# Optimization experiments

Measured on AMD Instinct MI355X. Metric: run time of the kernel, lower is better.

## Reference

```python
import jax, jax.numpy as jnp
import numpy as np

VOCAB = 32000
EMB = 128
HID = 256
NCLS = 8
B, S = 256, 512


def setup_inputs() -> dict:
    key = jax.random.key(0)
    ks = jax.random.split(key, 10)
    tokens = jax.random.randint(ks[0], (B, S), 0, VOCAB)
    emb = jax.random.normal(ks[1], (VOCAB, EMB), jnp.float32) * 0.02
    # LSTM params per direction: Wi [EMB,4H] (no bias, like flax dense_i),
    # Wh [H,4H] + bh [4H] (flax dense_h carries the bias). Gate order: i,f,g,o.
    si = 1.0 / np.sqrt(EMB)
    sh = 1.0 / np.sqrt(HID)
    Wi_f = jax.random.normal(ks[2], (EMB, 4 * HID), jnp.float32) * si
    Wh_f = jax.random.normal(ks[3], (HID, 4 * HID), jnp.float32) * sh
    b_f = jnp.zeros((4 * HID,), jnp.float32)
    Wi_b = jax.random.normal(ks[4], (EMB, 4 * HID), jnp.float32) * si
    Wh_b = jax.random.normal(ks[5], (HID, 4 * HID), jnp.float32) * sh
    b_b = jnp.zeros((4 * HID,), jnp.float32)
    Wd = jax.random.normal(ks[6], (2 * HID, NCLS), jnp.float32) * (1.0 / np.sqrt(2 * HID))
    bd = jnp.zeros((NCLS,), jnp.float32)
    return {"tokens": tokens, "emb": emb, "Wi_f": Wi_f, "Wh_f": Wh_f, "b_f": b_f,
            "Wi_b": Wi_b, "Wh_b": Wh_b, "b_b": b_b, "Wd": Wd, "bd": bd, "train": 0}


def _lstm_final_c(xs, Wi, Wh, bh):
    # xs: [B, S, E]. Returns final cell state c_S: [B, H].
    bsz = xs.shape[0]
    # Precompute input projections for all steps: [S, B, 4H]
    x_proj = jnp.einsum('bse,eg->sbg', xs, Wi) + bh

    def step(carry, xp_t):
        c, h = carry
        z = xp_t + h @ Wh  # [B, 4H]
        i, f, g, o = jnp.split(z, 4, axis=-1)
        c = jax.nn.sigmoid(f) * c + jax.nn.sigmoid(i) * jnp.tanh(g)
        h = jax.nn.sigmoid(o) * jnp.tanh(c)
        return (c, h), None

    init = (jnp.zeros((bsz, HID), xs.dtype), jnp.zeros((bsz, HID), xs.dtype))
    (c, h), _ = jax.lax.scan(step, init, x_proj)
    return c


def reference(tokens, emb, Wi_f, Wh_f, b_f, Wi_b, Wh_b, b_b, Wd, bd, train):
    x = emb[tokens]                       # [B, S, E]
    c_fwd = _lstm_final_c(x, Wi_f, Wh_f, b_f)
    c_bwd = _lstm_final_c(jnp.flip(x, axis=1), Wi_b, Wh_b, b_b)
    feat = jnp.concatenate([c_fwd, c_bwd], axis=-1)  # [B, 2H]
    # Dropout is deterministic (train=False) -> identity.
    return feat @ Wd + bd                 # [B, NCLS]
```

## Files before the change

kernel.cpp:

```cpp
#include <hip/hip_runtime.h>
#include <hip/hip_bf16.h>


typedef __attribute__((ext_vector_type(8))) short bf16x8;
typedef __attribute__((ext_vector_type(4))) float f32x4;

#define S_LEN 512

#define XF_OFF   0ULL
#define XF_SZ    (512ULL*16*4*64*16)
#define WHF_OFF  (XF_OFF + XF_SZ)
#define WHF_SZ   (2ULL*8*8*8*64*16)
#define WIF_OFF  (WHF_OFF + WHF_SZ)
#define WIF_SZ   (2ULL*8*4*8*64*16)
#define FEAT_OFF (WIF_OFF + WIF_SZ)
#define FEAT_SZ  (256ULL*512*4)
#define FLAG_OFF (FEAT_OFF + FEAT_SZ)
#define WS_NEED  (FLAG_OFF + 16)

__device__ __forceinline__ short f2bf(float f){
  union { float f; unsigned u; } v; v.f = f;
  unsigned u = v.u;
  u += 0x7fffu + ((u >> 16) & 1u);
  return (short)(u >> 16);
}
__device__ __forceinline__ float fsig(float x){
  float t = __builtin_amdgcn_exp2f(-1.44269504f * x);
  return __builtin_amdgcn_rcpf(1.0f + t);
}
__device__ __forceinline__ float ftanh(float x){
  float t = __builtin_amdgcn_exp2f(2.88539008f * x);
  return 1.0f - 2.0f * __builtin_amdgcn_rcpf(1.0f + t);
}
__device__ __forceinline__ int pack2(float a, float b){
  return (int)(unsigned short)f2bf(a) | ((int)(unsigned short)f2bf(b) << 16);
}
__device__ __forceinline__ int koff(int flag, int h, int j){
  return flag ? (8*h + j) : (j < 4 ? 4*h + j : 16 + 4*h + (j-4));
}
__device__ __forceinline__ bf16x8 loadA(const short* p, int colbase, int h, int flag){
  if (flag){
    return *(const bf16x8*)(p + colbase + 8*h);
  } else {
    short4 lo = *(const short4*)(p + colbase + 4*h);
    short4 hi = *(const short4*)(p + colbase + 16 + 4*h);
    bf16x8 r;
    r[0]=lo.x; r[1]=lo.y; r[2]=lo.z; r[3]=lo.w;
    r[4]=hi.x; r[5]=hi.y; r[6]=hi.z; r[7]=hi.w;
    return r;
  }
}

__device__ __noinline__ void spin_units(int n){
  float x = 1.5f;
  for (int i=0; i<n*300; i++) x = __builtin_amdgcn_rcpf(x + 1.0f);
  asm volatile("" :: "v"(x));
}
__global__ __launch_bounds__(64) void probe_kernel(char* ws){
  int l = threadIdx.x;
  float dref[4]; int n = l & 15;
  #pragma unroll
  for (int r=0;r<4;r++){
    int m = 4*(l>>4) + r; float s = 0.f;
    for (int k=0;k<32;k++)
      s += (0.25f*(float)((m*7+k*3)%5-2)) * (0.125f*(float)((k*5+n*11)%7-3));
    dref[r] = s;
  }
  f32x4 zero = {0.f,0.f,0.f,0.f};
  int bad[2];
  #pragma unroll
  for (int cand=0; cand<2; cand++){
    bf16x8 a, b;
    #pragma unroll
    for (int j=0;j<8;j++){
      int k = koff(cand, l>>4, j);
      a[j] = f2bf(0.25f*(float)(((l&15)*7+k*3)%5-2));
      b[j] = f2bf(0.125f*(float)((k*5+(l&15)*11)%7-3));
    }
    f32x4 d = __builtin_amdgcn_mfma_f32_16x16x32_bf16(a,b,zero,0,0,0);
    int bb = 0;
    #pragma unroll
    for (int r=0;r<4;r++) bb |= (fabsf(d[r]-dref[r]) > 1e-4f) ? 1 : 0;
    bad[cand] = bb;
  }
  unsigned long long B2 = __ballot(bad[1]);
  unsigned long long B1 = __ballot(bad[0]);
  if (l == 0){
    int flag = (B2 == 0ULL) ? 1 : 0;
    *(int*)(ws + FLAG_OFF) = flag;
  }
  if (B2) spin_units(10);
  if (B1) spin_units(30);
}

__global__ __launch_bounds__(256) void prep_kernel(const float* Wh_f, const float* Wh_b,
    const float* Wi_f, const float* Wi_b, char* ws){
  const int flag = *(const int*)(ws + FLAG_OFF);
  int gid = blockIdx.x*256 + threadIdx.x;
  if (blockIdx.x < 256){
    int e = gid;
    int lane = e&63, tl = (e>>6)&7, ks = (e>>9)&7, w = (e>>12)&7, dir = (e>>15)&1;
    const float* Wh = dir ? Wh_b : Wh_f;
    int G = tl>>1, nh = tl&1;
    int nn = G*256 + w*32 + nh*16 + (lane&15);
    int h = lane>>4, kb = ks*32;
    int kj[8];
    #pragma unroll
    for (int j=0;j<8;j++) kj[j] = kb + koff(flag, h, j);
    int4 pv;
    pv.x = pack2(Wh[kj[0]*1024+nn], Wh[kj[1]*1024+nn]);
    pv.y = pack2(Wh[kj[2]*1024+nn], Wh[kj[3]*1024+nn]);
    pv.z = pack2(Wh[kj[4]*1024+nn], Wh[kj[5]*1024+nn]);
    pv.w = pack2(Wh[kj[6]*1024+nn], Wh[kj[7]*1024+nn]);
    ((int4*)(ws + WHF_OFF))[e] = pv;
  } else {
    int e = gid - 65536;
    int lane = e&63, tl = (e>>6)&7, ks = (e>>9)&3, w = (e>>11)&7, dir = (e>>14)&1;
    const float* Wi = dir ? Wi_b : Wi_f;
    int G = tl>>1, nh = tl&1;
    int nn = G*256 + w*32 + nh*16 + (lane&15);
    int h = lane>>4, kb = ks*32;
    int kj[8];
    #pragma unroll
    for (int j=0;j<8;j++) kj[j] = kb + koff(flag, h, j);
    int4 pv;
    pv.x = pack2(Wi[kj[0]*1024+nn], Wi[kj[1]*1024+nn]);
    pv.y = pack2(Wi[kj[2]*1024+nn], Wi[kj[3]*1024+nn]);
    pv.z = pack2(Wi[kj[4]*1024+nn], Wi[kj[5]*1024+nn]);
    pv.w = pack2(Wi[kj[6]*1024+nn], Wi[kj[7]*1024+nn]);
    ((int4*)(ws + WIF_OFF))[e] = pv;
  }
}

__global__ __launch_bounds__(256) void embed_kernel(const int* tokens, const float* emb,
    char* ws){
  const int flag = *(const int*)(ws + FLAG_OFF);
  int e = blockIdx.x;
  int t = e >> 4, blk = e & 15;
  int tid = threadIdx.x;
  int ks = tid >> 6, lane = tid & 63;
  int h = lane >> 4, m = lane & 15;
  int b = blk*16 + m;
  int tok = tokens[b*S_LEN + t];
  const float* er = emb + (size_t)tok*128 + ks*32;
  float4 v0, v1;
  if (flag){
    v0 = *(const float4*)(er + 8*h);
    v1 = *(const float4*)(er + 8*h + 4);
  } else {
    v0 = *(const float4*)(er + 4*h);
    v1 = *(const float4*)(er + 16 + 4*h);
  }
  int4 pv;
  pv.x = pack2(v0.x,v0.y); pv.y = pack2(v0.z,v0.w);
  pv.z = pack2(v1.x,v1.y); pv.w = pack2(v1.z,v1.w);
  ((int4*)(ws + XF_OFF))[((size_t)e*4 + ks)*64 + lane] = pv;
}

__device__ __forceinline__ void lstm_step(
    int t, int dir, int blk, int w, int l, int flag,
    const int4* xf4, const int4* wif, const int4* whf,
    int4 (&xfUse)[4], int4 (&xfPre)[4],
    int4 (&bq)[3][8],
    const float (&bias)[8],
    const short* hRead, short* hWrite,
    float (&c)[8])
{
  int tn = (t+1 < S_LEN) ? t+1 : t;
  int tt = dir ? (S_LEN-1-tn) : tn;
  size_t xi = (((size_t)tt*16 + blk)*4)*64 + l;
  xfPre[0] = xf4[xi];     xfPre[1] = xf4[xi+64];
  xfPre[2] = xf4[xi+128]; xfPre[3] = xf4[xi+192];

  f32x4 acc[8];
  #pragma unroll
  for (int tl=0; tl<8; tl++){
    f32x4 v = {bias[tl],bias[tl],bias[tl],bias[tl]}; acc[tl] = v;
  }
  bf16x8 a[8];
  #pragma unroll
  for (int ks=0; ks<8; ks++)
    a[ks] = loadA(hRead + (l&15)*264, ks*32, l>>4, flag);

  #pragma unroll
  for (int cs=0; cs<12; cs++){
    bf16x8 af = (cs < 4) ? __builtin_bit_cast(bf16x8, xfUse[cs]) : a[cs-4];
    #pragma unroll
    for (int tl=0; tl<8; tl++)
      acc[tl] = __builtin_amdgcn_mfma_f32_16x16x32_bf16(af,
                  __builtin_bit_cast(bf16x8, bq[cs%3][tl]), acc[tl], 0,0,0);
    const int nc = (cs+3) % 12;
    const int4* src = (nc < 4) ? (wif + (size_t)(nc*8)*64)
                               : (whf + (size_t)((nc-4)*8)*64);
    #pragma unroll
    for (int tl=0; tl<8; tl++)
      bq[cs%3][tl] = src[(size_t)tl*64 + l];
  }
  #pragma unroll
  for (int nh=0; nh<2; nh++){
    #pragma unroll
    for (int r=0; r<4; r++){
      const int ci = nh*4 + r;
      float iv = acc[0+nh][r];
      float fv = acc[2+nh][r];
      float gv = acc[4+nh][r];
      float ov = acc[6+nh][r];
      float cc = fsig(fv)*c[ci] + fsig(iv)*ftanh(gv);
      c[ci] = cc;
      float hh = fsig(ov)*ftanh(cc);
      hWrite[(4*(l>>4)+r)*264 + w*32 + nh*16 + (l&15)] = f2bf(hh);
    }
  }
  __syncthreads();
}

__global__ __launch_bounds__(512,2) void rnn_kernel(const float* b_f, const float* b_b,
    char* ws){
  const int flag = *(const int*)(ws + FLAG_OFF);
  int bid = blockIdx.x; int dir = bid>>4, blk = bid&15;
  int tid = threadIdx.x; int w = tid>>6, l = tid&63;
  __shared__ short hbuf[2][16*264];
  for (int i=tid; i<16*264; i+=512) hbuf[0][i] = 0;
  const int4* xf4 = (const int4*)(ws + XF_OFF);
  const int4* whf = (const int4*)(ws + WHF_OFF) + ((size_t)dir*8 + w)*8*8*64;
  const int4* wif = (const int4*)(ws + WIF_OFF) + ((size_t)dir*8 + w)*4*8*64;
  float bias[8];
  {
    const float* bh = dir ? b_b : b_f;
    #pragma unroll
    for (int tl=0;tl<8;tl++){
      int G = tl>>1, nh = tl&1;
      bias[tl] = bh[G*256 + w*32 + nh*16 + (l&15)];
    }
  }
  float c[8] = {0,0,0,0,0,0,0,0};
  int4 xqA[4], xqB[4], bq[3][8];
  {
    int tt0 = dir ? (S_LEN-1) : 0;
    size_t xi0 = (((size_t)tt0*16 + blk)*4)*64 + l;
    xqA[0]=xf4[xi0];     xqA[1]=xf4[xi0+64];
    xqA[2]=xf4[xi0+128]; xqA[3]=xf4[xi0+192];
  }
  #pragma unroll
  for (int kp=0;kp<3;kp++)
    #pragma unroll
    for (int tl=0;tl<8;tl++) bq[kp][tl] = wif[(size_t)(kp*8+tl)*64 + l];
  __syncthreads();
  #pragma unroll 1
  for (int t=0; t<S_LEN; t+=2){
    lstm_step(t,   dir, blk, w, l, flag, xf4, wif, whf, xqA, xqB, bq, bias, hbuf[0], hbuf[1], c);
    lstm_step(t+1, dir, blk, w, l, flag, xf4, wif, whf, xqB, xqA, bq, bias, hbuf[1], hbuf[0], c);
  }
  float* feat = (float*)(ws + FEAT_OFF);
  #pragma unroll
  for (int nh=0; nh<2; nh++)
    #pragma unroll
    for (int r=0; r<4; r++)
      feat[((size_t)blk*16 + 4*(l>>4)+r)*512 + dir*256 + w*32 + nh*16 + (l&15)] = c[nh*4+r];
}

__global__ __launch_bounds__(256) void head_kernel(const float* Wd, const float* bd,
    const char* ws, float* out){
  __shared__ float wds[4096];
  int tid = threadIdx.x;
  for (int i=tid; i<4096; i+=256) wds[i] = Wd[i];
  __syncthreads();
  if (tid < 128){
    int row = blockIdx.x*16 + (tid>>3), col = tid&7;
    const float* fr = (const float*)(ws + FEAT_OFF) + (size_t)row*512;
    float s = bd[col];
    #pragma unroll 8
    for (int k=0;k<512;k++) s += fr[k]*wds[k*8+col];
    out[row*8+col] = s;
  }
}

extern "C" void kernel_launch(void* const* d_in, const int* in_sizes, int n_in,
                              void* d_out, int out_size, void* d_ws, size_t ws_size,
                              hipStream_t stream) {
  const int*   tokens = (const int*)d_in[0];
  const float* emb    = (const float*)d_in[1];
  const float* Wi_f   = (const float*)d_in[2];
  const float* Wh_f   = (const float*)d_in[3];
  const float* b_f    = (const float*)d_in[4];
  const float* Wi_b   = (const float*)d_in[5];
  const float* Wh_b   = (const float*)d_in[6];
  const float* b_b    = (const float*)d_in[7];
  const float* Wd     = (const float*)d_in[8];
  const float* bd     = (const float*)d_in[9];
  char* ws = (char*)d_ws;
  float* out = (float*)d_out;

  if (ws_size < WS_NEED) return;

  hipLaunchKernelGGL(probe_kernel, dim3(1),    dim3(64),  0, stream, ws);
  hipLaunchKernelGGL(prep_kernel,  dim3(384),  dim3(256), 0, stream, Wh_f, Wh_b, Wi_f, Wi_b, ws);
  hipLaunchKernelGGL(embed_kernel, dim3(8192), dim3(256), 0, stream, tokens, emb, ws);
  hipLaunchKernelGGL(rnn_kernel,   dim3(32),   dim3(512), 0, stream, b_f, b_b, ws);
  hipLaunchKernelGGL(head_kernel,  dim3(16),   dim3(256), 0, stream, Wd, bd, ws, out);
}
```

Before: 5.127 ms.

## Keep LSTM gate weights register-resident with 16 waves per block

The recurrent kernel goes from 8 to 16 waves per block, and each wave now owns 16 hidden columns across all four gates. This lets the whole bf16 Wi/Wh slice (48 int4 per lane) live in registers for all 512 steps instead of being re-streamed from global memory every step. The prep kernel is rewritten to emit the new per-wave layout. This removes the per-step weight load traffic, but it raises register pressure at 1024 threads per block and doubles the number of waves meeting at each step's barrier.

```diff
diff --git a/kernel.cpp b/kernel.cpp
--- a/kernel.cpp
+++ b/kernel.cpp
@@ -9,11 +9,9 @@
 
 #define XF_OFF   0ULL
 #define XF_SZ    (512ULL*16*4*64*16)
-#define WHF_OFF  (XF_OFF + XF_SZ)
-#define WHF_SZ   (2ULL*8*8*8*64*16)
-#define WIF_OFF  (WHF_OFF + WHF_SZ)
-#define WIF_SZ   (2ULL*8*4*8*64*16)
-#define FEAT_OFF (WIF_OFF + WIF_SZ)
+#define WF_OFF   (XF_OFF + XF_SZ)
+#define WF_SZ    (2ULL*16*12*4*64*16)
+#define FEAT_OFF (WF_OFF + WF_SZ)
 #define FEAT_SZ  (256ULL*512*4)
 #define FLAG_OFF (FEAT_OFF + FEAT_SZ)
 #define WS_NEED  (FLAG_OFF + 16)
@@ -96,40 +94,26 @@
 __global__ __launch_bounds__(256) void prep_kernel(const float* Wh_f, const float* Wh_b,
     const float* Wi_f, const float* Wi_b, char* ws){
   const int flag = *(const int*)(ws + FLAG_OFF);
-  int gid = blockIdx.x*256 + threadIdx.x;
-  if (blockIdx.x < 256){
-    int e = gid;
-    int lane = e&63, tl = (e>>6)&7, ks = (e>>9)&7, w = (e>>12)&7, dir = (e>>15)&1;
-    const float* Wh = dir ? Wh_b : Wh_f;
-    int G = tl>>1, nh = tl&1;
-    int nn = G*256 + w*32 + nh*16 + (lane&15);
-    int h = lane>>4, kb = ks*32;
-    int kj[8];
-    #pragma unroll
-    for (int j=0;j<8;j++) kj[j] = kb + koff(flag, h, j);
-    int4 pv;
-    pv.x = pack2(Wh[kj[0]*1024+nn], Wh[kj[1]*1024+nn]);
-    pv.y = pack2(Wh[kj[2]*1024+nn], Wh[kj[3]*1024+nn]);
-    pv.z = pack2(Wh[kj[4]*1024+nn], Wh[kj[5]*1024+nn]);
-    pv.w = pack2(Wh[kj[6]*1024+nn], Wh[kj[7]*1024+nn]);
-    ((int4*)(ws + WHF_OFF))[e] = pv;
-  } else {
-    int e = gid - 65536;
-    int lane = e&63, tl = (e>>6)&7, ks = (e>>9)&3, w = (e>>11)&7, dir = (e>>14)&1;
-    const float* Wi = dir ? Wi_b : Wi_f;
-    int G = tl>>1, nh = tl&1;
-    int nn = G*256 + w*32 + nh*16 + (lane&15);
-    int h = lane>>4, kb = ks*32;
-    int kj[8];
-    #pragma unroll
-    for (int j=0;j<8;j++) kj[j] = kb + koff(flag, h, j);
-    int4 pv;
-    pv.x = pack2(Wi[kj[0]*1024+nn], Wi[kj[1]*1024+nn]);
-    pv.y = pack2(Wi[kj[2]*1024+nn], Wi[kj[3]*1024+nn]);
-    pv.z = pack2(Wi[kj[4]*1024+nn], Wi[kj[5]*1024+nn]);
-    pv.w = pack2(Wi[kj[6]*1024+nn], Wi[kj[7]*1024+nn]);
-    ((int4*)(ws + WIF_OFF))[e] = pv;
-  }
+  int e = blockIdx.x*256 + threadIdx.x;
+  int lane = e&63;
+  int G = (e>>6)&3;
+  int q = e>>8;
+  int cs = q % 12, dw = q / 12;
+  int ww = dw & 15, dir = dw >> 4;
+  const float* W; int kb;
+  if (cs < 4){ W = dir ? Wi_b : Wi_f; kb = cs*32; }
+  else       { W = dir ? Wh_b : Wh_f; kb = (cs-4)*32; }
+  int nn = G*256 + ww*16 + (lane&15);
+  int h = lane>>4;
+  int kj[8];
+  #pragma unroll
+  for (int j=0;j<8;j++) kj[j] = kb + koff(flag, h, j);
+  int4 pv;
+  pv.x = pack2(W[kj[0]*1024+nn], W[kj[1]*1024+nn]);
+  pv.y = pack2(W[kj[2]*1024+nn], W[kj[3]*1024+nn]);
+  pv.z = pack2(W[kj[4]*1024+nn], W[kj[5]*1024+nn]);
+  pv.w = pack2(W[kj[6]*1024+nn], W[kj[7]*1024+nn]);
+  ((int4*)(ws + WF_OFF))[e] = pv;
 }
 
 __global__ __launch_bounds__(256) void embed_kernel(const int* tokens, const float* emb,
@@ -158,13 +142,13 @@
 }
 
 __device__ __forceinline__ void lstm_step(
-    int t, int dir, int blk, int w, int l, int flag,
-    const int4* xf4, const int4* wif, const int4* whf,
+    int t, int dir, int blk, int l, int flag, int hcol,
+    const int4* xf4,
+    const int4 (&wreg)[12][4],
     int4 (&xfUse)[4], int4 (&xfPre)[4],
-    int4 (&bq)[3][8],
-    const float (&bias)[8],
+    const float (&bias)[4],
     const short* hRead, short* hWrite,
-    float (&c)[8])
+    float (&c)[4])
 {
   int tn = (t+1 < S_LEN) ? t+1 : t;
   int tt = dir ? (S_LEN-1-tn) : tn;
@@ -172,10 +156,10 @@
   xfPre[0] = xf4[xi];     xfPre[1] = xf4[xi+64];
   xfPre[2] = xf4[xi+128]; xfPre[3] = xf4[xi+192];
 
-  f32x4 acc[8];
-  #pragma unroll
-  for (int tl=0; tl<8; tl++){
-    f32x4 v = {bias[tl],bias[tl],bias[tl],bias[tl]}; acc[tl] = v;
+  f32x4 acc[4];
+  #pragma unroll
+  for (int G=0; G<4; G++){
+    f32x4 v = {bias[G],bias[G],bias[G],bias[G]}; acc[G] = v;
   }
   bf16x8 a[8];
   #pragma unroll
@@ -186,77 +170,64 @@
   for (int cs=0; cs<12; cs++){
     bf16x8 af = (cs < 4) ? __builtin_bit_cast(bf16x8, xfUse[cs]) : a[cs-4];
     #pragma unroll
-    for (int tl=0; tl<8; tl++)
-      acc[tl] = __builtin_amdgcn_mfma_f32_16x16x32_bf16(af,
-                  __builtin_bit_cast(bf16x8, bq[cs%3][tl]), acc[tl], 0,0,0);
-    const int nc = (cs+3) % 12;
-    const int4* src = (nc < 4) ? (wif + (size_t)(nc*8)*64)
-                               : (whf + (size_t)((nc-4)*8)*64);
-    #pragma unroll
-    for (int tl=0; tl<8; tl++)
-      bq[cs%3][tl] = src[(size_t)tl*64 + l];
-  }
-  #pragma unroll
-  for (int nh=0; nh<2; nh++){
-    #pragma unroll
-    for (int r=0; r<4; r++){
-      const int ci = nh*4 + r;
-      float iv = acc[0+nh][r];
-      float fv = acc[2+nh][r];
-      float gv = acc[4+nh][r];
-      float ov = acc[6+nh][r];
-      float cc = fsig(fv)*c[ci] + fsig(iv)*ftanh(gv);
-      c[ci] = cc;
-      float hh = fsig(ov)*ftanh(cc);
-      hWrite[(4*(l>>4)+r)*264 + w*32 + nh*16 + (l&15)] = f2bf(hh);
-    }
+    for (int G=0; G<4; G++)
+      acc[G] = __builtin_amdgcn_mfma_f32_16x16x32_bf16(af,
+                 __builtin_bit_cast(bf16x8, wreg[cs][G]), acc[G], 0,0,0);
+  }
+  #pragma unroll
+  for (int r=0; r<4; r++){
+    float iv = acc[0][r];
+    float fv = acc[1][r];
+    float gv = acc[2][r];
+    float ov = acc[3][r];
+    float cc = fsig(fv)*c[r] + fsig(iv)*ftanh(gv);
+    c[r] = cc;
+    float hh = fsig(ov)*ftanh(cc);
+    hWrite[(4*(l>>4)+r)*264 + hcol] = f2bf(hh);
   }
   __syncthreads();
 }
 
-__global__ __launch_bounds__(512,2) void rnn_kernel(const float* b_f, const float* b_b,
+__global__ __launch_bounds__(1024) void rnn_kernel(const float* b_f, const float* b_b,
     char* ws){
   const int flag = *(const int*)(ws + FLAG_OFF);
   int bid = blockIdx.x; int dir = bid>>4, blk = bid&15;
-  int tid = threadIdx.x; int w = tid>>6, l = tid&63;
+  int tid = threadIdx.x; int ww = tid>>6, l = tid&63;
   __shared__ short hbuf[2][16*264];
-  for (int i=tid; i<16*264; i+=512) hbuf[0][i] = 0;
+  for (int i=tid; i<16*264; i+=1024) hbuf[0][i] = 0;
   const int4* xf4 = (const int4*)(ws + XF_OFF);
-  const int4* whf = (const int4*)(ws + WHF_OFF) + ((size_t)dir*8 + w)*8*8*64;
-  const int4* wif = (const int4*)(ws + WIF_OFF) + ((size_t)dir*8 + w)*4*8*64;
-  float bias[8];
+  const int4* wf  = (const int4*)(ws + WF_OFF) + ((size_t)(dir*16 + ww)*12*4)*64;
+  int4 wreg[12][4];
+  #pragma unroll
+  for (int cs=0; cs<12; cs++)
+    #pragma unroll
+    for (int G=0; G<4; G++)
+      wreg[cs][G] = wf[(size_t)(cs*4 + G)*64 + l];
+  float bias[4];
   {
     const float* bh = dir ? b_b : b_f;
     #pragma unroll
-    for (int tl=0;tl<8;tl++){
-      int G = tl>>1, nh = tl&1;
-      bias[tl] = bh[G*256 + w*32 + nh*16 + (l&15)];
-    }
-  }
-  float c[8] = {0,0,0,0,0,0,0,0};
-  int4 xqA[4], xqB[4], bq[3][8];
+    for (int G=0; G<4; G++) bias[G] = bh[G*256 + ww*16 + (l&15)];
+  }
+  int hcol = ww*16 + (l&15);
+  float c[4] = {0,0,0,0};
+  int4 xqA[4], xqB[4];
   {
     int tt0 = dir ? (S_LEN-1) : 0;
     size_t xi0 = (((size_t)tt0*16 + blk)*4)*64 + l;
     xqA[0]=xf4[xi0];     xqA[1]=xf4[xi0+64];
     xqA[2]=xf4[xi0+128]; xqA[3]=xf4[xi0+192];
   }
-  #pragma unroll
-  for (int kp=0;kp<3;kp++)
-    #pragma unroll
-    for (int tl=0;tl<8;tl++) bq[kp][tl] = wif[(size_t)(kp*8+tl)*64 + l];
   __syncthreads();
   #pragma unroll 1
   for (int t=0; t<S_LEN; t+=2){
-    lstm_step(t,   dir, blk, w, l, flag, xf4, wif, whf, xqA, xqB, bq, bias, hbuf[0], hbuf[1], c);
-    lstm_step(t+1, dir, blk, w, l, flag, xf4, wif, whf, xqB, xqA, bq, bias, hbuf[1], hbuf[0], c);
+    lstm_step(t,   dir, blk, l, flag, hcol, xf4, wreg, xqA, xqB, bias, hbuf[0], hbuf[1], c);
+    lstm_step(t+1, dir, blk, l, flag, hcol, xf4, wreg, xqB, xqA, bias, hbuf[1], hbuf[0], c);
   }
   float* feat = (float*)(ws + FEAT_OFF);
   #pragma unroll
-  for (int nh=0; nh<2; nh++)
-    #pragma unroll
-    for (int r=0; r<4; r++)
-      feat[((size_t)blk*16 + 4*(l>>4)+r)*512 + dir*256 + w*32 + nh*16 + (l&15)] = c[nh*4+r];
+  for (int r=0; r<4; r++)
+    feat[((size_t)blk*16 + 4*(l>>4)+r)*512 + dir*256 + hcol] = c[r];
 }
 
 __global__ __launch_bounds__(256) void head_kernel(const float* Wd, const float* bd,
@@ -293,9 +264,9 @@
 
   if (ws_size < WS_NEED) return;
 
-  hipLaunchKernelGGL(probe_kernel, dim3(1),    dim3(64),  0, stream, ws);
-  hipLaunchKernelGGL(prep_kernel,  dim3(384),  dim3(256), 0, stream, Wh_f, Wh_b, Wi_f, Wi_b, ws);
-  hipLaunchKernelGGL(embed_kernel, dim3(8192), dim3(256), 0, stream, tokens, emb, ws);
-  hipLaunchKernelGGL(rnn_kernel,   dim3(32),   dim3(512), 0, stream, b_f, b_b, ws);
-  hipLaunchKernelGGL(head_kernel,  dim3(16),   dim3(256), 0, stream, Wd, bd, ws, out);
-}
+  hipLaunchKernelGGL(probe_kernel, dim3(1),    dim3(64),   0, stream, ws);
+  hipLaunchKernelGGL(prep_kernel,  dim3(384),  dim3(256),  0, stream, Wh_f, Wh_b, Wi_f, Wi_b, ws);
+  hipLaunchKernelGGL(embed_kernel, dim3(8192), dim3(256),  0, stream, tokens, emb, ws);
+  hipLaunchKernelGGL(rnn_kernel,   dim3(32),   dim3(1024), 0, stream, b_f, b_b, ws);
+  hipLaunchKernelGGL(head_kernel,  dim3(16),   dim3(256),  0, stream, Wd, bd, ws, out);
+}
```

Result: slower. 10.12 ms (+97.4%).
